# Kernel optimization log

Measured on AMD Instinct MI355X. Metric: run time of the kernel, lower is better.

Reference implementation:

```python
import jax, jax.numpy as jnp
import numpy as np

BETA = 0.25  # commitment loss weight


def setup_inputs() -> dict:
    key = jax.random.key(0)
    k1, k2 = jax.random.split(key)
    z = jax.random.normal(k1, (16, 256, 64, 64), dtype=jnp.float32)      # encoder latent, NCHW
    codebook = jax.random.normal(k2, (1024, 256), dtype=jnp.float32)     # [n_e, e_dim]
    return {"z": z, "codebook": codebook}


def reference(z, codebook):
    B, C, H, W = z.shape
    z_bhwc = jnp.transpose(z, (0, 2, 3, 1))            # [B,H,W,C]
    zf = z_bhwc.reshape(-1, C)                          # [N,C], N = B*H*W
    # squared L2 distance to every codeword: ||z||^2 + ||e||^2 - 2 z.e
    d = ((zf * zf).sum(axis=1, keepdims=True)
         + (codebook * codebook).sum(axis=1)[None, :]
         - 2.0 * zf @ codebook.T)                       # [N, n_e]
    idx = jnp.argmin(d, axis=1)                         # [N] nearest codeword
    zq = codebook[idx].reshape(B, H, W, C)              # irregular gather
    # VQ loss: codebook term + beta * commitment term
    loss = (BETA * jnp.mean((jax.lax.stop_gradient(zq) - z_bhwc) ** 2)
            + jnp.mean((zq - jax.lax.stop_gradient(z_bhwc)) ** 2))
    # straight-through estimator
    zq_st = z_bhwc + jax.lax.stop_gradient(zq - z_bhwc)
    return jnp.transpose(zq_st, (0, 3, 1, 2)), loss
```

## Files before the change

### kernel.cpp

```cpp
#include <hip/hip_runtime.h>
#include <cfloat>

#define C_DIM 256
#define HW    4096
#define NE    1024
#define NPIX  65536
#define TAU   0.15f
#define ZSTR  264

typedef __attribute__((ext_vector_type(8))) _Float16 half8_t;
typedef __attribute__((ext_vector_type(4))) float floatx4;

__device__ __forceinline__ unsigned int fenc(float f) {
  unsigned int u = __float_as_uint(f);
  return (u & 0x80000000u) ? ~u : (u | 0x80000000u);
}


__global__ __launch_bounds__(256)
void prep_kernel(const float* __restrict__ cb, _Float16* __restrict__ EhfP,
                 float* __restrict__ e2, float* __restrict__ acc,
                 int* __restrict__ ccount) {
  if (blockIdx.x < 128) {
    const int g = blockIdx.x >> 3, it = blockIdx.x & 7;
    const int sidx = it * 256 + (int)threadIdx.x;
    const int ks = sidx >> 8, i = (sidx >> 6) & 3, lane = sidx & 63;
    const int ln = lane & 15, quad = lane >> 4;
    const float* src = cb + (size_t)(g * 64 + i * 16 + ln) * C_DIM + ks * 32 + quad * 8;
    const float4 v0 = *(const float4*)(src);
    const float4 v1 = *(const float4*)(src + 4);
    half8_t h;
    h[0] = (_Float16)v0.x; h[1] = (_Float16)v0.y; h[2] = (_Float16)v0.z; h[3] = (_Float16)v0.w;
    h[4] = (_Float16)v1.x; h[5] = (_Float16)v1.y; h[6] = (_Float16)v1.z; h[7] = (_Float16)v1.w;
    *(half8_t*)(EhfP + (size_t)g * 16384 + (size_t)sidx * 8) = h;
  } else {
    if (blockIdx.x == 128 && threadIdx.x == 0) { acc[0] = 0.f; ccount[0] = 0; }
    const int bid = blockIdx.x - 128;
    const int wave = (bid * 256 + (int)threadIdx.x) >> 6;
    const int lane = threadIdx.x & 63;
    const float4 v = *(const float4*)(cb + (size_t)wave * C_DIM + lane * 4);
    float s = v.x * v.x + v.y * v.y + v.z * v.z + v.w * v.w;
    #pragma unroll
    for (int off = 32; off; off >>= 1) s += __shfl_down(s, off, 64);
    if (lane == 0) e2[wave] = s;
  }
}

__global__ __launch_bounds__(256, 2)
void screen_kernel(const float* __restrict__ z, const _Float16* __restrict__ EhfP,
                   const float* __restrict__ e2, const float* __restrict__ cb,
                   int* __restrict__ clist, int* __restrict__ ccount,
                   float* __restrict__ acc_out, float* __restrict__ out) {
  __shared__ __align__(16) _Float16 Zl[128 * ZSTR];
  __shared__ float e2l[NE];

  const int tid = threadIdx.x;
  const int ptile = blockIdx.x * 128;
  const int b = ptile >> 12, pb = ptile & 4095;
  const float* zb = z + (size_t)b * (C_DIM * HW) + pb;

  float s_z2 = 0.f;
  #pragma unroll
  for (int it = 0; it < 16; ++it) {
    const int flat = it * 256 + tid;
    const int p = flat & 127, kb = flat >> 7;
    float f[8];
    #pragma unroll
    for (int j = 0; j < 8; ++j) f[j] = zb[(size_t)(kb * 8 + j) * HW + p];
    half8_t h;
    #pragma unroll
    for (int j = 0; j < 8; ++j) { s_z2 = fmaf(f[j], f[j], s_z2); h[j] = (_Float16)f[j]; }
    *(half8_t*)&Zl[p * ZSTR + kb * 8] = h;
  }
  #pragma unroll
  for (int i = 0; i < 4; ++i) e2l[i * 256 + tid] = e2[i * 256 + tid];
  __syncthreads();

  const int lane = tid & 63;
  const int w = tid >> 6;
  const int wc = w & 1, wp = w >> 1;
  const int ln = lane & 15, quad = lane >> 4;

  const _Float16* aBase = EhfP + (size_t)wc * 16384 + (size_t)lane * 8;
  const char* rowB[4];
  #pragma unroll
  for (int j = 0; j < 4; ++j)
    rowB[j] = (const char*)(&Zl[(wp * 64 + j * 16 + ln) * ZSTR + quad * 8]);

  float d1[4], d2[4]; int i1[4];
  #pragma unroll
  for (int j = 0; j < 4; ++j) { d1[j] = FLT_MAX; d2[j] = FLT_MAX; i1[j] = 0; }

  half8_t abuf[2][4], bbuf[2][4];
  #pragma unroll
  for (int i = 0; i < 4; ++i) abuf[0][i] = *(const half8_t*)(aBase + i * 512);
  #pragma unroll
  for (int j = 0; j < 4; ++j) bbuf[0][j] = *(const half8_t*)(rowB[j]);

  for (int nc = 0; nc < 8; ++nc) {
    floatx4 acc[4][4];
    #pragma unroll
    for (int i = 0; i < 4; ++i)
      #pragma unroll
      for (int j = 0; j < 4; ++j) acc[i][j] = (floatx4){0.f, 0.f, 0.f, 0.f};

    #pragma unroll
    for (int ks = 0; ks < 8; ++ks) {
      const int cur = ks & 1, nxt = cur ^ 1;
      const int s1 = nc * 8 + ks + 1;
      const int sp = s1 > 63 ? 63 : s1;
      const size_t aoff = (size_t)(sp >> 3) * 32768 + (size_t)(sp & 7) * 2048;
      const int bks = sp & 7;
      #pragma unroll
      for (int i = 0; i < 4; ++i) abuf[nxt][i] = *(const half8_t*)(aBase + aoff + i * 512);
      #pragma unroll
      for (int j = 0; j < 4; ++j) bbuf[nxt][j] = *(const half8_t*)(rowB[j] + bks * 64);
      __builtin_amdgcn_s_setprio(1);
      #pragma unroll
      for (int i = 0; i < 4; ++i)
        #pragma unroll
        for (int j = 0; j < 4; ++j)
          acc[i][j] = __builtin_amdgcn_mfma_f32_16x16x32_f16(abuf[cur][i], bbuf[cur][j], acc[i][j], 0, 0, 0);
      __builtin_amdgcn_s_setprio(0);
    }

    const int cwb = nc * 128 + wc * 64;
    #pragma unroll
    for (int i = 0; i < 4; ++i) {
      const int cw0 = cwb + i * 16 + quad * 4;
      float ee[4];
      #pragma unroll
      for (int r = 0; r < 4; ++r) ee[r] = e2l[cw0 + r];
      #pragma unroll
      for (int j = 0; j < 4; ++j) {
        #pragma unroll
        for (int r = 0; r < 4; ++r) {
          const float d = fmaf(-2.0f, acc[i][j][r], ee[r]);
          const bool lt = d < d1[j];
          const float hi = lt ? d1[j] : d;
          d1[j] = lt ? d : d1[j];
          i1[j] = lt ? (cw0 + r) : i1[j];
          d2[j] = fminf(d2[j], hi);
        }
      }
    }
  }

  #pragma unroll
  for (int j = 0; j < 4; ++j) {
    #pragma unroll
    for (int m = 16; m <= 32; m <<= 1) {
      const float od1 = __shfl_xor(d1[j], m, 64);
      const int   oi1 = __shfl_xor(i1[j], m, 64);
      const float od2 = __shfl_xor(d2[j], m, 64);
      const bool take = (od1 < d1[j]) || (od1 == d1[j] && oi1 < i1[j]);
      const float hi = take ? d1[j] : od1;
      d1[j] = take ? od1 : d1[j];
      i1[j] = take ? oi1 : i1[j];
      d2[j] = fminf(fminf(d2[j], od2), hi);
    }
  }

  __syncthreads();
  float* rd1  = (float*)Zl;
  int*   ri1  = (int*)Zl + 256;
  float* rd2  = (float*)Zl + 512;
  float* zsq  = (float*)Zl + 768;
  float* dsum = (float*)Zl + 1024;
  int*   fid  = (int*)Zl + 1152;
  if (lane < 16) {
    #pragma unroll
    for (int j = 0; j < 4; ++j) {
      const int p = wp * 64 + j * 16 + ln;
      rd1[wc * 128 + p] = d1[j];
      ri1[wc * 128 + p] = i1[j];
      rd2[wc * 128 + p] = d2[j];
    }
  }
  zsq[tid] = s_z2;
  __syncthreads();
  if (tid < 128) {
    const float a1 = rd1[tid], b1 = rd1[128 + tid];
    const int   ai = ri1[tid], bi = ri1[128 + tid];
    const float a2 = rd2[tid], b2 = rd2[128 + tid];
    const bool take = (b1 < a1) || (b1 == a1 && bi < ai);
    const float d1f = take ? b1 : a1;
    const int   i1f = take ? bi : ai;
    const float hi  = take ? a1 : b1;
    const float d2f = fminf(fminf(a2, b2), hi);
    fid[tid]  = i1f;
    dsum[tid] = d1f;
    if ((d2f - d1f) <= TAU) {
      const int pos = atomicAdd(ccount, 1);
      clist[pos] = ptile + tid;
    }
  }
  __syncthreads();
  if (tid < 64) {
    float v = zsq[tid] + zsq[tid + 64] + zsq[tid + 128] + zsq[tid + 192]
            + dsum[tid] + dsum[tid + 64];
    #pragma unroll
    for (int off = 32; off; off >>= 1) v += __shfl_down(v, off, 64);
    if (tid == 0) atomicAdd(acc_out, v);
  }
  {
    const int pl = tid & 127, cs = tid >> 7;
    const int id = fid[pl];
    const float* er = cb + (size_t)id * C_DIM + cs * 128;
    float* orow = out + (size_t)b * (C_DIM * HW) + (size_t)(cs * 128) * HW + pb + pl;
    #pragma unroll 8
    for (int c = 0; c < 128; c += 4) {
      const float4 ev = *(const float4*)(er + c);
      orow[(size_t)(c + 0) * HW] = ev.x;
      orow[(size_t)(c + 1) * HW] = ev.y;
      orow[(size_t)(c + 2) * HW] = ev.z;
      orow[(size_t)(c + 3) * HW] = ev.w;
    }
  }
}

__global__ __launch_bounds__(256)
void rescan_kernel(const float* __restrict__ z, const float* __restrict__ cb,
                   const float* __restrict__ e2, const int* __restrict__ clist,
                   const int* __restrict__ ccount, float* __restrict__ out,
                   const float* __restrict__ acc, float* __restrict__ loss_out) {
  if (blockIdx.x == 0 && threadIdx.x == 0)
    *loss_out = 1.25f * (*acc) * (1.0f / 16777216.0f);
  __shared__ __align__(16) float zl[4][C_DIM];
  __shared__ int pxs[4];
  __shared__ unsigned long long bestk[4];
  const int n = *ccount;
  const int ngroups = (n + 3) >> 2;
  for (int g = blockIdx.x; g < ngroups; g += gridDim.x) {
    const int base = g * 4;
    if ((int)threadIdx.x < 4) {
      pxs[threadIdx.x] = clist[min(base + (int)threadIdx.x, n - 1)];
      bestk[threadIdx.x] = ~0ULL;
    }
    __syncthreads();
    {
      const int k = threadIdx.x;
      #pragma unroll
      for (int i = 0; i < 4; ++i) {
        const int gp = pxs[i];
        zl[i][k] = z[(size_t)(gp >> 12) * (C_DIM * HW) + (size_t)k * HW + (gp & 4095)];
      }
    }
    __syncthreads();
    unsigned long long mykey[4] = {~0ULL, ~0ULL, ~0ULL, ~0ULL};
    #pragma unroll 1
    for (int o = 0; o < 4; ++o) {
      const int cw = o * 256 + (int)threadIdx.x;
      const float* row = cb + (size_t)cw * C_DIM;
      float dot[4] = {0.f, 0.f, 0.f, 0.f};
      #pragma unroll 4
      for (int k0 = 0; k0 < C_DIM; k0 += 4) {
        const float4 ev = *(const float4*)(row + k0);
        #pragma unroll
        for (int i = 0; i < 4; ++i) {
          const float4 zz = *(const float4*)&zl[i][k0];
          dot[i] = fmaf(ev.x, zz.x, dot[i]);
          dot[i] = fmaf(ev.y, zz.y, dot[i]);
          dot[i] = fmaf(ev.z, zz.z, dot[i]);
          dot[i] = fmaf(ev.w, zz.w, dot[i]);
        }
      }
      const float ee = e2[cw];
      #pragma unroll
      for (int i = 0; i < 4; ++i) {
        const float d = fmaf(-2.0f, dot[i], ee);
        const unsigned long long key = ((unsigned long long)fenc(d) << 32) | (unsigned)cw;
        mykey[i] = key < mykey[i] ? key : mykey[i];
      }
    }
    #pragma unroll
    for (int i = 0; i < 4; ++i) {
      unsigned long long k = mykey[i];
      #pragma unroll
      for (int off = 32; off; off >>= 1) {
        const unsigned long long ok = __shfl_xor(k, off, 64);
        k = ok < k ? ok : k;
      }
      if ((threadIdx.x & 63) == 0) atomicMin(&bestk[i], k);
    }
    __syncthreads();
    {
      const int i = (int)threadIdx.x >> 6;
      const int l = (int)threadIdx.x & 63;
      const int gp = pxs[i];
      const int id = (int)(unsigned)(bestk[i] & 0xFFFFFFFFull);
      const float* er = cb + (size_t)id * C_DIM;
      float* orow = out + (size_t)(gp >> 12) * (C_DIM * HW) + (gp & 4095);
      const float4 ev = *(const float4*)(er + l * 4);
      orow[(size_t)(l * 4 + 0) * HW] = ev.x;
      orow[(size_t)(l * 4 + 1) * HW] = ev.y;
      orow[(size_t)(l * 4 + 2) * HW] = ev.z;
      orow[(size_t)(l * 4 + 3) * HW] = ev.w;
    }
    __syncthreads();
  }
}

extern "C" void kernel_launch(void* const* d_in, const int* in_sizes, int n_in,
                              void* d_out, int out_size, void* d_ws, size_t ws_size,
                              hipStream_t stream) {
  const float* z  = (const float*)d_in[0];
  const float* cb = (const float*)d_in[1];
  float* out = (float*)d_out;
  char* ws = (char*)d_ws;

  float*    acc    = (float*)ws;
  int*      ccount = (int*)(ws + 8);
  float*    e2     = (float*)(ws + 4096);
  _Float16* EhfP   = (_Float16*)(ws + 8192);
  int*      clist  = (int*)(ws + 532480);

  prep_kernel<<<384, 256, 0, stream>>>(cb, EhfP, e2, acc, ccount);
  screen_kernel<<<NPIX / 128, 256, 0, stream>>>(z, EhfP, e2, cb, clist, ccount, acc, out);
  rescan_kernel<<<1024, 256, 0, stream>>>(z, cb, e2, clist, ccount, out, acc,
                                          out + 16777216);
}
```

Before: 193.4 us.

## Enlarge screen tile to 256 pixels with 512 threads and 4x8 MFMA per wave

```diff
diff --git a/kernel.cpp b/kernel.cpp
--- a/kernel.cpp
+++ b/kernel.cpp
@@ -46,24 +46,24 @@
   }
 }
 
-__global__ __launch_bounds__(256, 2)
+__global__ __launch_bounds__(512, 2)
 void screen_kernel(const float* __restrict__ z, const _Float16* __restrict__ EhfP,
                    const float* __restrict__ e2, const float* __restrict__ cb,
                    int* __restrict__ clist, int* __restrict__ ccount,
                    float* __restrict__ acc_out, float* __restrict__ out) {
-  __shared__ __align__(16) _Float16 Zl[128 * ZSTR];
+  __shared__ __align__(16) _Float16 Zl[256 * ZSTR];
   __shared__ float e2l[NE];
 
   const int tid = threadIdx.x;
-  const int ptile = blockIdx.x * 128;
+  const int ptile = blockIdx.x * 256;
   const int b = ptile >> 12, pb = ptile & 4095;
   const float* zb = z + (size_t)b * (C_DIM * HW) + pb;
 
   float s_z2 = 0.f;
   #pragma unroll
   for (int it = 0; it < 16; ++it) {
-    const int flat = it * 256 + tid;
-    const int p = flat & 127, kb = flat >> 7;
+    const int flat = it * 512 + tid;
+    const int p = flat & 255, kb = flat >> 8;
     float f[8];
     #pragma unroll
     for (int j = 0; j < 8; ++j) f[j] = zb[(size_t)(kb * 8 + j) * HW + p];
@@ -73,58 +73,55 @@
     *(half8_t*)&Zl[p * ZSTR + kb * 8] = h;
   }
   #pragma unroll
-  for (int i = 0; i < 4; ++i) e2l[i * 256 + tid] = e2[i * 256 + tid];
+  for (int i = 0; i < 2; ++i) e2l[i * 512 + tid] = e2[i * 512 + tid];
   __syncthreads();
 
   const int lane = tid & 63;
   const int w = tid >> 6;
-  const int wc = w & 1, wp = w >> 1;
+  const int wc = w & 3, wp = w >> 2;
   const int ln = lane & 15, quad = lane >> 4;
 
   const _Float16* aBase = EhfP + (size_t)wc * 16384 + (size_t)lane * 8;
-  const char* rowB[4];
-  #pragma unroll
-  for (int j = 0; j < 4; ++j)
-    rowB[j] = (const char*)(&Zl[(wp * 64 + j * 16 + ln) * ZSTR + quad * 8]);
-
-  float d1[4], d2[4]; int i1[4];
-  #pragma unroll
-  for (int j = 0; j < 4; ++j) { d1[j] = FLT_MAX; d2[j] = FLT_MAX; i1[j] = 0; }
-
-  half8_t abuf[2][4], bbuf[2][4];
+  const char* rowB[8];
+  #pragma unroll
+  for (int j = 0; j < 8; ++j)
+    rowB[j] = (const char*)(&Zl[(wp * 128 + j * 16 + ln) * ZSTR + quad * 8]);
+
+  float d1[8], d2[8]; int i1[8];
+  #pragma unroll
+  for (int j = 0; j < 8; ++j) { d1[j] = FLT_MAX; d2[j] = FLT_MAX; i1[j] = 0; }
+
+  half8_t abuf[2][4], bbuf[8];
   #pragma unroll
   for (int i = 0; i < 4; ++i) abuf[0][i] = *(const half8_t*)(aBase + i * 512);
-  #pragma unroll
-  for (int j = 0; j < 4; ++j) bbuf[0][j] = *(const half8_t*)(rowB[j]);
-
-  for (int nc = 0; nc < 8; ++nc) {
-    floatx4 acc[4][4];
+
+  for (int nc = 0; nc < 4; ++nc) {
+    floatx4 acc[4][8];
     #pragma unroll
     for (int i = 0; i < 4; ++i)
       #pragma unroll
-      for (int j = 0; j < 4; ++j) acc[i][j] = (floatx4){0.f, 0.f, 0.f, 0.f};
+      for (int j = 0; j < 8; ++j) acc[i][j] = (floatx4){0.f, 0.f, 0.f, 0.f};
 
     #pragma unroll
     for (int ks = 0; ks < 8; ++ks) {
-      const int cur = ks & 1, nxt = cur ^ 1;
-      const int s1 = nc * 8 + ks + 1;
-      const int sp = s1 > 63 ? 63 : s1;
-      const size_t aoff = (size_t)(sp >> 3) * 32768 + (size_t)(sp & 7) * 2048;
-      const int bks = sp & 7;
+      const int s = nc * 8 + ks;
+      const int cur = s & 1, nxt = cur ^ 1;
+      #pragma unroll
+      for (int j = 0; j < 8; ++j) bbuf[j] = *(const half8_t*)(rowB[j] + ks * 64);
+      const int sp = s + 1 > 31 ? 31 : s + 1;
+      const size_t aoff = (size_t)(sp >> 3) * 65536 + (size_t)(sp & 7) * 2048;
       #pragma unroll
       for (int i = 0; i < 4; ++i) abuf[nxt][i] = *(const half8_t*)(aBase + aoff + i * 512);
-      #pragma unroll
-      for (int j = 0; j < 4; ++j) bbuf[nxt][j] = *(const half8_t*)(rowB[j] + bks * 64);
       __builtin_amdgcn_s_setprio(1);
       #pragma unroll
       for (int i = 0; i < 4; ++i)
         #pragma unroll
-        for (int j = 0; j < 4; ++j)
-          acc[i][j] = __builtin_amdgcn_mfma_f32_16x16x32_f16(abuf[cur][i], bbuf[cur][j], acc[i][j], 0, 0, 0);
+        for (int j = 0; j < 8; ++j)
+          acc[i][j] = __builtin_amdgcn_mfma_f32_16x16x32_f16(abuf[cur][i], bbuf[j], acc[i][j], 0, 0, 0);
       __builtin_amdgcn_s_setprio(0);
     }
 
-    const int cwb = nc * 128 + wc * 64;
+    const int cwb = nc * 256 + wc * 64;
     #pragma unroll
     for (int i = 0; i < 4; ++i) {
       const int cw0 = cwb + i * 16 + quad * 4;
@@ -132,7 +129,7 @@
       #pragma unroll
       for (int r = 0; r < 4; ++r) ee[r] = e2l[cw0 + r];
       #pragma unroll
-      for (int j = 0; j < 4; ++j) {
+      for (int j = 0; j < 8; ++j) {
         #pragma unroll
         for (int r = 0; r < 4; ++r) {
           const float d = fmaf(-2.0f, acc[i][j][r], ee[r]);
@@ -147,7 +144,7 @@
   }
 
   #pragma unroll
-  for (int j = 0; j < 4; ++j) {
+  for (int j = 0; j < 8; ++j) {
     #pragma unroll
     for (int m = 16; m <= 32; m <<= 1) {
       const float od1 = __shfl_xor(d1[j], m, 64);
@@ -163,48 +160,56 @@
 
   __syncthreads();
   float* rd1  = (float*)Zl;
-  int*   ri1  = (int*)Zl + 256;
-  float* rd2  = (float*)Zl + 512;
-  float* zsq  = (float*)Zl + 768;
-  float* dsum = (float*)Zl + 1024;
-  int*   fid  = (int*)Zl + 1152;
+  int*   ri1  = (int*)Zl + 1024;
+  float* rd2  = (float*)Zl + 2048;
+  float* zsq  = (float*)Zl + 3072;
+  float* dsum = (float*)Zl + 3584;
+  int*   fid  = (int*)Zl + 3840;
   if (lane < 16) {
     #pragma unroll
-    for (int j = 0; j < 4; ++j) {
-      const int p = wp * 64 + j * 16 + ln;
-      rd1[wc * 128 + p] = d1[j];
-      ri1[wc * 128 + p] = i1[j];
-      rd2[wc * 128 + p] = d2[j];
+    for (int j = 0; j < 8; ++j) {
+      const int p = wp * 128 + j * 16 + ln;
+      rd1[wc * 256 + p] = d1[j];
+      ri1[wc * 256 + p] = i1[j];
+      rd2[wc * 256 + p] = d2[j];
     }
   }
   zsq[tid] = s_z2;
   __syncthreads();
-  if (tid < 128) {
-    const float a1 = rd1[tid], b1 = rd1[128 + tid];
-    const int   ai = ri1[tid], bi = ri1[128 + tid];
-    const float a2 = rd2[tid], b2 = rd2[128 + tid];
-    const bool take = (b1 < a1) || (b1 == a1 && bi < ai);
-    const float d1f = take ? b1 : a1;
-    const int   i1f = take ? bi : ai;
-    const float hi  = take ? a1 : b1;
-    const float d2f = fminf(fminf(a2, b2), hi);
-    fid[tid]  = i1f;
-    dsum[tid] = d1f;
-    if ((d2f - d1f) <= TAU) {
+  if (tid < 256) {
+    float a1 = rd1[tid]; int ai = ri1[tid]; float a2 = rd2[tid];
+    #pragma unroll
+    for (int m = 1; m < 4; ++m) {
+      const float b1 = rd1[m * 256 + tid];
+      const int   bi = ri1[m * 256 + tid];
+      const float b2 = rd2[m * 256 + tid];
+      const bool take = (b1 < a1) || (b1 == a1 && bi < ai);
+      const float hi = take ? a1 : b1;
+      a1 = take ? b1 : a1;
+      ai = take ? bi : ai;
+      a2 = fminf(fminf(a2, b2), hi);
+    }
+    const int gp = ptile + tid;
+    fid[tid]  = ai;
+    dsum[tid] = a1;
+    if ((a2 - a1) <= TAU) {
       const int pos = atomicAdd(ccount, 1);
-      clist[pos] = ptile + tid;
+      clist[pos] = gp;
     }
   }
   __syncthreads();
   if (tid < 64) {
-    float v = zsq[tid] + zsq[tid + 64] + zsq[tid + 128] + zsq[tid + 192]
-            + dsum[tid] + dsum[tid + 64];
+    float v = 0.f;
+    #pragma unroll
+    for (int k = 0; k < 8; ++k) v += zsq[tid + k * 64];
+    #pragma unroll
+    for (int k = 0; k < 4; ++k) v += dsum[tid + k * 64];
     #pragma unroll
     for (int off = 32; off; off >>= 1) v += __shfl_down(v, off, 64);
     if (tid == 0) atomicAdd(acc_out, v);
   }
   {
-    const int pl = tid & 127, cs = tid >> 7;
+    const int pl = tid & 255, cs = tid >> 8;
     const int id = fid[pl];
     const float* er = cb + (size_t)id * C_DIM + cs * 128;
     float* orow = out + (size_t)b * (C_DIM * HW) + (size_t)(cs * 128) * HW + pb + pl;
@@ -316,7 +321,7 @@
   int*      clist  = (int*)(ws + 532480);
 
   prep_kernel<<<384, 256, 0, stream>>>(cb, EhfP, e2, acc, ccount);
-  screen_kernel<<<NPIX / 128, 256, 0, stream>>>(z, EhfP, e2, cb, clist, ccount, acc, out);
+  screen_kernel<<<NPIX / 256, 512, 0, stream>>>(z, EhfP, e2, cb, clist, ccount, acc, out);
   rescan_kernel<<<1024, 256, 0, stream>>>(z, cb, e2, clist, ccount, out, acc,
                                           out + 16777216);
 }
```

After: 329.9 us. 1.71x slower.
